# Kernel optimization log

Hardware: AMD Instinct MI355X
Metric: run time of the kernel (lower is better)

The kernel has to match this reference:

```python
import jax, jax.numpy as jnp
import numpy as np

D_MODEL = 1024
H = 16
D_K = D_MODEL // H
D_FF = 4096
EPS = 1e-5
NEG = -1e9


def setup_inputs() -> dict:
    key = jax.random.key(0)
    ks = jax.random.split(key, 12)
    B, S = 4, 1024
    s = 1.0 / np.sqrt(D_MODEL)
    inp = {
        'x': jax.random.normal(ks[0], (B, S, D_MODEL), dtype=jnp.float32),
        'src_mask': jax.random.randint(ks[1], (B, 1, 1, S), 0, 2, dtype=jnp.int32),
        'wq': jax.random.normal(ks[2], (D_MODEL, D_MODEL), dtype=jnp.float32) * s,
        'bq': jnp.zeros((D_MODEL,), jnp.float32),
        'wk': jax.random.normal(ks[3], (D_MODEL, D_MODEL), dtype=jnp.float32) * s,
        'bk': jnp.zeros((D_MODEL,), jnp.float32),
        'wv': jax.random.normal(ks[4], (D_MODEL, D_MODEL), dtype=jnp.float32) * s,
        'bv': jnp.zeros((D_MODEL,), jnp.float32),
        'wo': jax.random.normal(ks[5], (D_MODEL, D_MODEL), dtype=jnp.float32) * s,
        'bo': jnp.zeros((D_MODEL,), jnp.float32),
        'w1': jax.random.normal(ks[6], (D_MODEL, D_FF), dtype=jnp.float32) * s,
        'b1': jnp.zeros((D_FF,), jnp.float32),
        'w2': jax.random.normal(ks[7], (D_FF, D_MODEL), dtype=jnp.float32) * (1.0 / np.sqrt(D_FF)),
        'b2': jnp.zeros((D_MODEL,), jnp.float32),
        'ln1_a': jnp.ones((1,), jnp.float32),
        'ln1_b': jnp.zeros((1,), jnp.float32),
        'ln2_a': jnp.ones((1,), jnp.float32),
        'ln2_b': jnp.zeros((1,), jnp.float32),
    }
    return inp


def _layernorm(x, alpha, bias):
    # Matches torch: mean over last dim; std is UNBIASED (ddof=1); divide by (std + eps).
    mean = jnp.mean(x, axis=-1, keepdims=True)
    std = jnp.sqrt(jnp.var(x, axis=-1, keepdims=True, ddof=1))
    return alpha * (x - mean) / (std + EPS) + bias


def _attention(xn, src_mask, wq, bq, wk, bk, wv, bv, wo, bo):
    B, S, _ = xn.shape
    q = (xn @ wq + bq).reshape(B, S, H, D_K).transpose(0, 2, 1, 3)  # [B,H,S,Dk]
    k = (xn @ wk + bk).reshape(B, S, H, D_K).transpose(0, 2, 1, 3)
    v = (xn @ wv + bv).reshape(B, S, H, D_K).transpose(0, 2, 1, 3)
    scores = jnp.einsum('bhqd,bhkd->bhqk', q, k) / np.sqrt(D_K)
    scores = jnp.where(src_mask == 0, NEG, scores)
    # NOTE: original module applies NO softmax (faithful to source).
    out = jnp.einsum('bhqk,bhkd->bhqd', scores, v)  # [B,H,S,Dk]
    out = out.transpose(0, 2, 1, 3).reshape(B, S, D_MODEL)
    return out @ wo + bo


def reference(x, src_mask, wq, bq, wk, bk, wv, bv, wo, bo,
              w1, b1, w2, b2, ln1_a, ln1_b, ln2_a, ln2_b):
    # Pre-norm residual 1: self-attention
    x = x + _attention(_layernorm(x, ln1_a, ln1_b), src_mask,
                       wq, bq, wk, bk, wv, bv, wo, bo)
    # Pre-norm residual 2: FFN
    xn = _layernorm(x, ln2_a, ln2_b)
    ffn = jax.nn.relu(xn @ w1 + b1) @ w2 + b2
    return x + ffn
```

## Files before the change

### kernel.cpp

```cpp
#include <hip/hip_runtime.h>
#include <hip/hip_bf16.h>
#include <math.h>


#define EPS 1e-5f

typedef __attribute__((ext_vector_type(8))) short bf16x8;
typedef __attribute__((ext_vector_type(4))) float f32x4;
typedef __attribute__((ext_vector_type(8))) int i32x8;
typedef __attribute__((ext_vector_type(4))) int i32x4;

typedef const __attribute__((address_space(1))) unsigned char glob_byte;
typedef __attribute__((address_space(3))) unsigned char lds_byte;

__device__ __forceinline__ void g2l16(const void* g, void* l) {
  __builtin_amdgcn_global_load_lds((glob_byte*)g, (lds_byte*)l, 16, 0, 0);
}

__device__ __forceinline__ unsigned short f2bf(float f) {
  union { float f; unsigned int u; } v; v.f = f;
  return (unsigned short)((v.u + 0x7FFFu + ((v.u >> 16) & 1u)) >> 16);
}
__device__ __forceinline__ float bf2f(unsigned short b) {
  union { unsigned int u; float f; } v; v.u = (unsigned int)b << 16;
  return v.f;
}
__device__ __forceinline__ unsigned int pk_fp8x4(float a, float b, float c, float d) {
  unsigned int p = 0;
  p = __builtin_amdgcn_cvt_pk_fp8_f32(a, b, p, false);
  p = __builtin_amdgcn_cvt_pk_fp8_f32(c, d, p, true);
  return p;
}
__device__ __forceinline__ unsigned char f2f8(float v) {
  return (unsigned char)(__builtin_amdgcn_cvt_pk_fp8_f32(v, v, 0, false) & 0xFF);
}

__global__ __launch_bounds__(256) void wconv_ln_kernel(
    const float* __restrict__ wq, const float* __restrict__ wk,
    const float* __restrict__ wv, const float* __restrict__ wo,
    const float* __restrict__ w1, const float* __restrict__ w2,
    const float* __restrict__ bq, const float* __restrict__ bk,
    const float* __restrict__ bv, const float* __restrict__ bo,
    unsigned char* __restrict__ wqkvF8, unsigned short* __restrict__ woT,
    unsigned short* __restrict__ wvT16,
    unsigned char* __restrict__ w1F8, unsigned char* __restrict__ w2F8,
    float* __restrict__ bqkv, float* __restrict__ cboW,
    const float* __restrict__ x, unsigned char* __restrict__ xnF8,
    unsigned short* __restrict__ xn16,
    const float* __restrict__ ln1a, const float* __restrict__ ln1b) {
  __shared__ float tile[64][65];
  const int bid = blockIdx.x;
  const int t = threadIdx.x;
  if (bid >= 3073) {
    const int row = bid - 3073;
    const float4 v = ((const float4*)(x + (size_t)row * 1024))[t];
    float s  = v.x + v.y + v.z + v.w;
    float ss = v.x * v.x + v.y * v.y + v.z * v.z + v.w * v.w;
#pragma unroll
    for (int off = 32; off > 0; off >>= 1) {
      s  += __shfl_down(s, off, 64);
      ss += __shfl_down(ss, off, 64);
    }
    __shared__ float red[8];
    const int lane = t & 63, wv_ = t >> 6;
    if (lane == 0) { red[wv_] = s; red[4 + wv_] = ss; }
    __syncthreads();
    const float S  = red[0] + red[1] + red[2] + red[3];
    const float SS = red[4] + red[5] + red[6] + red[7];
    const float mean = S * (1.0f / 1024.0f);
    float var = (SS - 1024.0f * mean * mean) * (1.0f / 1023.0f);
    var = fmaxf(var, 0.0f);
    const float scl = ln1a[0] / (sqrtf(var) + EPS);
    const float b = ln1b[0];
    const float o0 = (v.x - mean) * scl + b;
    const float o1 = (v.y - mean) * scl + b;
    const float o2 = (v.z - mean) * scl + b;
    const float o3 = (v.w - mean) * scl + b;
    ((unsigned int*)xnF8)[(size_t)row * 256 + t] = pk_fp8x4(o0, o1, o2, o3);
    ushort4 o4;
    o4.x = f2bf(o0); o4.y = f2bf(o1); o4.z = f2bf(o2); o4.w = f2bf(o3);
    ((ushort4*)(xn16 + (size_t)row * 1024))[t] = o4;
    return;
  }
  if (bid == 3072) {
#pragma unroll
    for (int i = 0; i < 12; ++i) {
      const int n = i * 256 + t;
      bqkv[n] = n < 1024 ? bq[n] : (n < 2048 ? bk[n - 1024] : bv[n - 2048]);
    }
#pragma unroll
    for (int i = 0; i < 16; ++i) {
      const int idx = i * 256 + t;
      cboW[idx] = bo[idx & 1023];
    }
    return;
  }
  const float* src; int K, N, tk, tn;
  unsigned short* dst16 = nullptr; unsigned char* dst8 = nullptr;
  unsigned short* dstv = nullptr;
  if (bid < 1024) {
    const int m = bid >> 8, loc = bid & 255;
    src = m == 0 ? wq : m == 1 ? wk : m == 2 ? wv : wo;
    if (m == 3) dst16 = woT;
    else { dst8 = wqkvF8 + (size_t)m * 1024 * 1024; if (m == 2) dstv = wvT16; }
    K = 1024; N = 1024; tk = loc >> 4; tn = loc & 15;
  } else if (bid < 2048) {
    const int loc = bid - 1024; src = w1; dst8 = w1F8;
    K = 1024; N = 4096; tk = loc >> 6; tn = loc & 63;
  } else {
    const int loc = bid - 2048; src = w2; dst8 = w2F8;
    K = 4096; N = 1024; tk = loc >> 4; tn = loc & 15;
  }
  const int lr = t >> 4, lc = (t & 15) * 4;
#pragma unroll
  for (int i = 0; i < 4; ++i) {
    const float4 v = *(const float4*)(src + (size_t)(tk * 64 + lr + 16 * i) * N + tn * 64 + lc);
    tile[lr + 16 * i][lc + 0] = v.x;
    tile[lr + 16 * i][lc + 1] = v.y;
    tile[lr + 16 * i][lc + 2] = v.z;
    tile[lr + 16 * i][lc + 3] = v.w;
  }
  __syncthreads();
  const int on = t >> 2, ok = (t & 3) * 16;
#pragma unroll
  for (int jj = 0; jj < 4; ++jj) {
    if (dst8) {
      const unsigned int p = pk_fp8x4(tile[ok + 4 * jj + 0][on], tile[ok + 4 * jj + 1][on],
                                      tile[ok + 4 * jj + 2][on], tile[ok + 4 * jj + 3][on]);
      *(unsigned int*)(dst8 + (size_t)(tn * 64 + on) * K + tk * 64 + ok + 4 * jj) = p;
      if (dstv) {
        ushort4 o4;
        o4.x = f2bf(tile[ok + 4 * jj + 0][on]);
        o4.y = f2bf(tile[ok + 4 * jj + 1][on]);
        o4.z = f2bf(tile[ok + 4 * jj + 2][on]);
        o4.w = f2bf(tile[ok + 4 * jj + 3][on]);
        *(ushort4*)(dstv + (size_t)(tn * 64 + on) * 1024 + tk * 64 + ok + 4 * jj) = o4;
      }
    } else {
      ushort4 o4;
      o4.x = f2bf(tile[ok + 4 * jj + 0][on]);
      o4.y = f2bf(tile[ok + 4 * jj + 1][on]);
      o4.z = f2bf(tile[ok + 4 * jj + 2][on]);
      o4.w = f2bf(tile[ok + 4 * jj + 3][on]);
      *(ushort4*)(dst16 + (size_t)(tn * 64 + on) * K + tk * 64 + ok + 4 * jj) = o4;
    }
  }
}

__global__ __launch_bounds__(256) void msum_kernel(
    const unsigned short* __restrict__ xn16, const int* __restrict__ mask,
    float* __restrict__ partials, float* __restrict__ nmp) {
  const int blk = blockIdx.x, b = blk >> 4, rc = blk & 15;
  const int t = threadIdx.x;
  const int row0 = b * 1024 + rc * 64;
  float4 s = {0.f, 0.f, 0.f, 0.f};
  float cnt = 0.f;
#pragma unroll 4
  for (int r = 0; r < 64; ++r) {
    const int row = row0 + r;
    if (mask[row] == 0) {
      const ushort4 v = ((const ushort4*)(xn16 + (size_t)row * 1024))[t];
      s.x += bf2f(v.x); s.y += bf2f(v.y); s.z += bf2f(v.z); s.w += bf2f(v.w);
      cnt += 1.f;
    }
  }
  ((float4*)(partials + (size_t)blk * 1024))[t] = s;
  if (t == 0) nmp[blk] = cnt;
}

template <int EPI, int TN, int RX, int RY>
__global__ __launch_bounds__(256, 4) void mfma_gemm_fp8(
    const unsigned char* __restrict__ A, const unsigned char* __restrict__ Bt,
    const float* __restrict__ bias, const void* __restrict__ resv,
    void* __restrict__ C0, void* __restrict__ C1, const int* __restrict__ maskG,
    int N, int lda, int ldb, int KH) {
  constexpr int NSPAN = TN / 2;
  constexpr int NJ = NSPAN / 16;
  __shared__ __align__(16) unsigned char As[128 * 128];
  __shared__ __align__(16) unsigned char Bs[TN * 128];
  const int tid = threadIdx.x, lane = tid & 63;
  const int w = tid >> 6;
  const int quad = lane >> 4, col = lane & 15;
  const int wm = w & 1, wn = w >> 1;

  int bx = blockIdx.x, by = blockIdx.y;
  {
    const int gx = gridDim.x;
    const int L = bx + gx * by;
    const int r = L & 7, s = L >> 3;
    const int nrx = gx / RX;
    const int rx = r % nrx, ry = r / nrx;
    bx = rx * RX + s % RX;
    by = ry * RY + (s / RX) % RY;
  }
  const int m0 = by * 128, n0 = bx * TN;
  if (EPI == 3) {
    const int bb = m0 >> 10;
    Bt += (size_t)bb * 1024 * ldb;
    bias += bb * 1024;
  }

  f32x4 acc[4][NJ];
  const f32x4 z4 = {0.f, 0.f, 0.f, 0.f};
#pragma unroll
  for (int i = 0; i < 4; ++i)
#pragma unroll
    for (int j = 0; j < NJ; ++j) acc[i][j] = z4;

  for (int k0 = 0; k0 < KH; k0 += 128) {
    __syncthreads();
#pragma unroll
    for (int t = 0; t < 4; ++t) {
      const int s = t * 256 + tid;
      const int r = s >> 3, c = (s & 7) ^ (r & 7);
      g2l16(A + (size_t)(m0 + r) * lda + k0 + c * 16, (void*)(As + s * 16));
    }
#pragma unroll
    for (int t = 0; t < TN / 32; ++t) {
      const int s = t * 256 + tid;
      const int r = s >> 3, c = (s & 7) ^ (r & 7);
      g2l16(Bt + (size_t)(n0 + r) * ldb + k0 + c * 16, (void*)(Bs + s * 16));
    }
    __syncthreads();
    i32x8 af[4];
#pragma unroll
    for (int i = 0; i < 4; ++i) {
      const int rr = wm * 64 + i * 16 + col;
      const i32x4* rowp = (const i32x4*)(As + rr * 128);
      const i32x4 lo = rowp[(2 * quad) ^ (rr & 7)];
      const i32x4 hi = rowp[(2 * quad + 1) ^ (rr & 7)];
      af[i] = __builtin_shufflevector(lo, hi, 0, 1, 2, 3, 4, 5, 6, 7);
    }
#pragma unroll
    for (int j = 0; j < NJ; ++j) {
      const int rr = wn * NSPAN + j * 16 + col;
      const i32x4* rowp = (const i32x4*)(Bs + rr * 128);
      const i32x4 lo = rowp[(2 * quad) ^ (rr & 7)];
      const i32x4 hi = rowp[(2 * quad + 1) ^ (rr & 7)];
      const i32x8 bfj = __builtin_shufflevector(lo, hi, 0, 1, 2, 3, 4, 5, 6, 7);
#pragma unroll
      for (int i = 0; i < 4; ++i)
        acc[i][j] = __builtin_amdgcn_mfma_scale_f32_16x16x128_f8f6f4(
            af[i], bfj, acc[i][j], 0, 0, 0, 0x7F7F7F7Fu, 0, 0x7F7F7F7Fu);
    }
  }
#pragma unroll
  for (int i = 0; i < 4; ++i) {
    const int mrow = m0 + wm * 64 + i * 16 + quad * 4;
#pragma unroll
    for (int j = 0; j < NJ; ++j) {
      const int n = n0 + wn * NSPAN + j * 16 + col;
      const float bn = bias[n];
      if (EPI == 2) {
        if (n0 >= 1024) {
          float v0 = acc[i][j][0] + bn;
          float v1 = acc[i][j][1] + bn;
          float v2 = acc[i][j][2] + bn;
          float v3 = acc[i][j][3] + bn;
          if (n0 < 2048) {
            const int4 mq = *(const int4*)(maskG + mrow);
            v0 = mq.x ? v0 : 0.f;
            v1 = mq.y ? v1 : 0.f;
            v2 = mq.z ? v2 : 0.f;
            v3 = mq.w ? v3 : 0.f;
          }
          *(unsigned int*)((unsigned char*)C1 + (size_t)(n - 1024) * 4096 + mrow) =
              pk_fp8x4(v0, v1, v2, v3);
        } else {
#pragma unroll
          for (int r = 0; r < 4; ++r)
            ((unsigned char*)C0)[(size_t)(mrow + r) * N + n] = f2f8(acc[i][j][r] + bn);
        }
        continue;
      }
#pragma unroll
      for (int r = 0; r < 4; ++r) {
        const int m = mrow + r;
        if (EPI == 0) {
          ((unsigned char*)C0)[(size_t)m * N + n] = f2f8(fmaxf(acc[i][j][r] + bn, 0.f));
        } else if (EPI == 1) {
          const float v = acc[i][j][r] + bn + bf2f(((const unsigned short*)resv)[(size_t)m * N + n]);
          ((float*)C0)[(size_t)m * N + n] = v;
        } else {
          const float v = acc[i][j][r] + bn + ((const float*)resv)[(size_t)m * N + n];
          ((unsigned short*)C0)[(size_t)m * N + n] = f2bf(v);
        }
      }
    }
  }
}

__global__ __launch_bounds__(256) void ln2_kernel(
    const unsigned short* __restrict__ x1,
    const float* __restrict__ alpha, const float* __restrict__ beta,
    unsigned char* __restrict__ xn2f8) {
  const int row = blockIdx.x, t = threadIdx.x;
  const size_t i = (size_t)row * 256 + t;
  const ushort4 a4 = ((const ushort4*)x1)[i];
  float4 v;
  v.x = bf2f(a4.x); v.y = bf2f(a4.y); v.z = bf2f(a4.z); v.w = bf2f(a4.w);
  float s  = v.x + v.y + v.z + v.w;
  float ss = v.x * v.x + v.y * v.y + v.z * v.z + v.w * v.w;
#pragma unroll
  for (int off = 32; off > 0; off >>= 1) {
    s  += __shfl_down(s, off, 64);
    ss += __shfl_down(ss, off, 64);
  }
  __shared__ float red[8];
  const int lane = t & 63, wv_ = t >> 6;
  if (lane == 0) { red[wv_] = s; red[4 + wv_] = ss; }
  __syncthreads();
  const float S  = red[0] + red[1] + red[2] + red[3];
  const float SS = red[4] + red[5] + red[6] + red[7];
  const float mean = S * (1.0f / 1024.0f);
  float var = (SS - 1024.0f * mean * mean) * (1.0f / 1023.0f);
  var = fmaxf(var, 0.0f);
  const float scl = alpha[0] / (sqrtf(var) + EPS);
  const float bb = beta[0];
  ((unsigned int*)xn2f8)[i] = pk_fp8x4((v.x - mean) * scl + bb,
                                       (v.y - mean) * scl + bb,
                                       (v.z - mean) * scl + bb,
                                       (v.w - mean) * scl + bb);
}

__global__ __launch_bounds__(512) void moment_kernel(
    const unsigned char* __restrict__ kvT8, const unsigned short* __restrict__ woT,
    const unsigned short* __restrict__ wvT16, const float* __restrict__ bqkv,
    const float* __restrict__ partials, const float* __restrict__ nmp,
    unsigned char* __restrict__ Wbt8, float* __restrict__ cboW) {
  __shared__ __align__(16) unsigned char Ks[64 * 512];
  __shared__ __align__(16) unsigned char Vs[64 * 512];
  __shared__ __align__(16) unsigned short Ms[64 * 64];
  __shared__ float sS[1024];
  __shared__ float corrS[64];
  const int tid = threadIdx.x, lane = tid & 63, w = tid >> 6;
  const int quad = lane >> 4, col = lane & 15;
  const int bh = blockIdx.x, b = bh >> 4, h = bh & 15;
  const int w4 = w & 3, ch = w >> 2;
  const f32x4 z4 = {0.f, 0.f, 0.f, 0.f};
  const size_t kb = (size_t)(h * 64) * 4096 + b * 1024;
  const size_t vb = (size_t)(1024 + h * 64) * 4096 + b * 1024;

#pragma unroll
  for (int i = 0; i < 4; ++i) {
    const int s = i * 512 + tid;
    const int r = s >> 5, c = (s & 31) ^ (r & 31);
    g2l16(kvT8 + kb + (size_t)r * 4096 + c * 16, (void*)(Ks + s * 16));
    g2l16(kvT8 + vb + (size_t)r * 4096 + c * 16, (void*)(Vs + s * 16));
  }
  {
    float2 sacc = {0.f, 0.f};
#pragma unroll
    for (int rc = 0; rc < 16; ++rc) {
      const float2 p = ((const float2*)(partials + (size_t)(b * 16 + rc) * 1024))[tid];
      sacc.x += p.x; sacc.y += p.y;
    }
    ((float2*)sS)[tid] = sacc;
  }
  float nm = 0.f;
#pragma unroll
  for (int i = 0; i < 16; ++i) nm += nmp[b * 16 + i];
  __syncthreads();

  {
    const int d2 = tid >> 3, kq = tid & 7;
    const unsigned short* wrow = wvT16 + (size_t)(h * 64 + d2) * 1024 + kq * 128;
    float s = 0.f;
#pragma unroll
    for (int jj = 0; jj < 16; ++jj) {
      const bf16x8 w8 = *(const bf16x8*)(wrow + jj * 8);
      const float* sp = sS + kq * 128 + jj * 8;
      s += bf2f((unsigned short)w8[0]) * sp[0] + bf2f((unsigned short)w8[1]) * sp[1] +
           bf2f((unsigned short)w8[2]) * sp[2] + bf2f((unsigned short)w8[3]) * sp[3] +
           bf2f((unsigned short)w8[4]) * sp[4] + bf2f((unsigned short)w8[5]) * sp[5] +
           bf2f((unsigned short)w8[6]) * sp[6] + bf2f((unsigned short)w8[7]) * sp[7];
    }
    s += __shfl_xor(s, 1, 64);
    s += __shfl_xor(s, 2, 64);
    s += __shfl_xor(s, 4, 64);
    if ((lane & 7) == 0) corrS[d2] = s + nm * bqkv[2048 + h * 64 + d2];
  }

  f32x4 acc[2] = {z4, z4};
  const int rr = w4 * 16 + col;
#pragma unroll 1
  for (int st = 0; st < 2; ++st) {
    if (st) {
      __syncthreads();
#pragma unroll
      for (int i = 0; i < 4; ++i) {
        const int s = i * 512 + tid;
        const int r = s >> 5, c = (s & 31) ^ (r & 31);
        g2l16(kvT8 + kb + (size_t)r * 4096 + 512 + c * 16, (void*)(Ks + s * 16));
        g2l16(kvT8 + vb + (size_t)r * 4096 + 512 + c * 16, (void*)(Vs + s * 16));
      }
      __syncthreads();
    }
#pragma unroll
    for (int q = 0; q < 4; ++q) {
      const i32x4* rowpK = (const i32x4*)(Ks + rr * 512);
      const i32x4 klo = rowpK[(q * 8 + 2 * quad) ^ (rr & 31)];
      const i32x4 khi = rowpK[(q * 8 + 2 * quad + 1) ^ (rr & 31)];
      const i32x8 af = __builtin_shufflevector(klo, khi, 0, 1, 2, 3, 4, 5, 6, 7);
#pragma unroll
      for (int cl = 0; cl < 2; ++cl) {
        const int vr = (ch * 2 + cl) * 16 + col;
        const i32x4* rowpV = (const i32x4*)(Vs + vr * 512);
        const i32x4 vlo = rowpV[(q * 8 + 2 * quad) ^ (vr & 31)];
        const i32x4 vhi = rowpV[(q * 8 + 2 * quad + 1) ^ (vr & 31)];
        const i32x8 vf = __builtin_shufflevector(vlo, vhi, 0, 1, 2, 3, 4, 5, 6, 7);
        acc[cl] = __builtin_amdgcn_mfma_scale_f32_16x16x128_f8f6f4(
            af, vf, acc[cl], 0, 0, 0, 0x7F7F7F7Fu, 0, 0x7F7F7F7Fu);
      }
    }
  }
#pragma unroll
  for (int cl = 0; cl < 2; ++cl) {
    const int d2 = (ch * 2 + cl) * 16 + col;
#pragma unroll
    for (int r = 0; r < 4; ++r) {
      const int d1 = w4 * 16 + quad * 4 + r;
      Ms[d1 * 64 + ((d2 >> 3) ^ (d1 & 7)) * 8 + (d2 & 7)] = f2bf(0.125f * acc[cl][r]);
    }
  }
  __syncthreads();

  unsigned char* Wb8 = Wbt8 + (size_t)b * 1048576;
#pragma unroll 1
  for (int nt8 = 0; nt8 < 8; ++nt8) {
    const int nbase = (w * 8 + nt8) * 16;
    const bf16x8 af0 = *(const bf16x8*)(woT + (size_t)(nbase + col) * 1024 + h * 64 + quad * 8);
    const bf16x8 af1 = *(const bf16x8*)(woT + (size_t)(nbase + col) * 1024 + h * 64 + 32 + quad * 8);
#pragma unroll
    for (int dt = 0; dt < 4; ++dt) {
      const int d1r = dt * 16 + col;
      const bf16x8 bf0 = *(const bf16x8*)(Ms + d1r * 64 + ((quad ^ (d1r & 7)) * 8));
      const bf16x8 bf1 = *(const bf16x8*)(Ms + d1r * 64 + (((4 + quad) ^ (d1r & 7)) * 8));
      f32x4 a = __builtin_amdgcn_mfma_f32_16x16x32_bf16(af0, bf0, z4, 0, 0, 0);
      a = __builtin_amdgcn_mfma_f32_16x16x32_bf16(af1, bf1, a, 0, 0, 0);
#pragma unroll
      for (int r = 0; r < 4; ++r)
        Wb8[(size_t)(nbase + quad * 4 + r) * 1024 + h * 64 + dt * 16 + col] = f2f8(a[r]);
    }
  }
#pragma unroll
  for (int rep = 0; rep < 2; ++rep) {
    const int n = rep * 512 + tid;
    const unsigned short* wrow = woT + (size_t)n * 1024 + h * 64;
    float s = 0.f;
#pragma unroll
    for (int k = 0; k < 64; k += 8) {
      const bf16x8 w8 = *(const bf16x8*)(wrow + k);
      s += bf2f((unsigned short)w8[0]) * corrS[k + 0] +
           bf2f((unsigned short)w8[1]) * corrS[k + 1] +
           bf2f((unsigned short)w8[2]) * corrS[k + 2] +
           bf2f((unsigned short)w8[3]) * corrS[k + 3] +
           bf2f((unsigned short)w8[4]) * corrS[k + 4] +
           bf2f((unsigned short)w8[5]) * corrS[k + 5] +
           bf2f((unsigned short)w8[6]) * corrS[k + 6] +
           bf2f((unsigned short)w8[7]) * corrS[k + 7];
    }
    atomicAdd(cboW + b * 1024 + n, -1e9f * s);
  }
}

extern "C" void kernel_launch(void* const* d_in, const int* in_sizes, int n_in,
                              void* d_out, int out_size, void* d_ws, size_t ws_size,
                              hipStream_t stream) {
  const float* x    = (const float*)d_in[0];
  const int*   mask = (const int*)d_in[1];
  const float* wq = (const float*)d_in[2];
  const float* bq = (const float*)d_in[3];
  const float* wk = (const float*)d_in[4];
  const float* bk = (const float*)d_in[5];
  const float* wv = (const float*)d_in[6];
  const float* bv = (const float*)d_in[7];
  const float* wo = (const float*)d_in[8];
  const float* bo = (const float*)d_in[9];
  const float* w1 = (const float*)d_in[10];
  const float* b1 = (const float*)d_in[11];
  const float* w2 = (const float*)d_in[12];
  const float* b2 = (const float*)d_in[13];
  const float* ln1a = (const float*)d_in[14];
  const float* ln1b = (const float*)d_in[15];
  const float* ln2a = (const float*)d_in[16];
  const float* ln2b = (const float*)d_in[17];
  float* out = (float*)d_out;
  char* W = (char*)d_ws;
  const size_t MB = 1u << 20;

  unsigned char*  wqkvF8 = (unsigned char*)(W + 0 * MB);
  unsigned short* woT    = (unsigned short*)(W + 3 * MB);
  unsigned short* wvT16  = (unsigned short*)(W + 5 * MB);
  unsigned char*  w1F8   = (unsigned char*)(W + 7 * MB);
  unsigned char*  w2F8   = (unsigned char*)(W + 11 * MB);
  float*          bqkv   = (float*)(W + 15 * MB);
  float*          cboW   = (float*)(W + 15 * MB + 65536);
  float*          partials = (float*)(W + 15 * MB + 131072);
  float*          nmp    = (float*)(W + 15 * MB + 393216);
  unsigned char*  xnF8   = (unsigned char*)(W + 16 * MB);
  unsigned char*  Q8     = (unsigned char*)(W + 20 * MB);
  unsigned char*  kvT8   = (unsigned char*)(W + 24 * MB);
  unsigned char*  Wbt8   = (unsigned char*)(W + 32 * MB);
  unsigned short* x1     = (unsigned short*)(W + 36 * MB);
  unsigned short* xn16   = (unsigned short*)(W + 44 * MB);
  unsigned char*  xn2f8  = (unsigned char*)(W + 52 * MB);
  unsigned char*  hbF8   = (unsigned char*)(W + 56 * MB);

  wconv_ln_kernel<<<7169, 256, 0, stream>>>(wq, wk, wv, wo, w1, w2, bq, bk, bv, bo,
                                            wqkvF8, woT, wvT16, w1F8, w2F8,
                                            bqkv, cboW, x, xnF8, xn16, ln1a, ln1b);
  msum_kernel<<<64, 256, 0, stream>>>(xn16, mask, partials, nmp);
  mfma_gemm_fp8<2, 128, 12, 8><<<dim3(24, 32), 256, 0, stream>>>(
      xnF8, wqkvF8, bqkv, nullptr, Q8, kvT8, mask, 1024, 1024, 1024, 1024);
  moment_kernel<<<64, 512, 0, stream>>>(kvT8, woT, wvT16, bqkv, partials, nmp,
                                        Wbt8, cboW);
  mfma_gemm_fp8<3, 64, 8, 8><<<dim3(16, 32), 256, 0, stream>>>(
      Q8, Wbt8, cboW, x, x1, nullptr, nullptr, 1024, 1024, 1024, 1024);
  ln2_kernel<<<4096, 256, 0, stream>>>(x1, ln2a, ln2b, xn2f8);
  mfma_gemm_fp8<0, 128, 16, 8><<<dim3(32, 32), 256, 0, stream>>>(
      xn2f8, w1F8, b1, nullptr, hbF8, nullptr, nullptr, 4096, 1024, 1024, 1024);
  mfma_gemm_fp8<1, 64, 8, 8><<<dim3(16, 32), 256, 0, stream>>>(
      hbF8, w2F8, b2, x1, out, nullptr, nullptr, 1024, 4096, 4096, 4096);
}
```

Measured before the change: 266.3 us.

## Quantize QKV, FFN weights and activations to FP4 for scaled MFMA GEMMs

Replaces the FP8 operand encoding for the QKV projection and both FFN GEMMs with a hand-rolled FP4 (e2m1) encoder. Weights are pre-scaled by 32 or 64 and the scale is undone through the MFMA block-scale argument. The GEMM kernel is duplicated into an FP4 variant that packs two k-steps per LDS tile, halving operand bytes and load traffic. The FFN hidden activation is also stored packed in FP4. This heavily reduces numeric precision of activations and weights, which risks accuracy-tolerance failures.

```diff
diff --git a/kernel.cpp b/kernel.cpp
--- a/kernel.cpp
+++ b/kernel.cpp
@@ -33,6 +33,14 @@
 }
 __device__ __forceinline__ unsigned char f2f8(float v) {
   return (unsigned char)(__builtin_amdgcn_cvt_pk_fp8_f32(v, v, 0, false) & 0xFF);
+}
+__device__ __forceinline__ unsigned fp4enc(float v) {
+  const float a = fabsf(v);
+  unsigned c = (unsigned)(a >= 0.25f) + (unsigned)(a >= 0.75f) +
+               (unsigned)(a >= 1.25f) + (unsigned)(a >= 1.75f) +
+               (unsigned)(a >= 2.5f) + (unsigned)(a >= 3.5f) +
+               (unsigned)(a >= 5.0f);
+  return c | (v < 0.f ? 8u : 0u);
 }
 
 __global__ __launch_bounds__(256) void wconv_ln_kernel(
@@ -41,11 +49,11 @@
     const float* __restrict__ w1, const float* __restrict__ w2,
     const float* __restrict__ bq, const float* __restrict__ bk,
     const float* __restrict__ bv, const float* __restrict__ bo,
-    unsigned char* __restrict__ wqkvF8, unsigned short* __restrict__ woT,
+    unsigned char* __restrict__ wqkvF4, unsigned short* __restrict__ woT,
     unsigned short* __restrict__ wvT16,
-    unsigned char* __restrict__ w1F8, unsigned char* __restrict__ w2F8,
+    unsigned char* __restrict__ w1F4, unsigned char* __restrict__ w2F4,
     float* __restrict__ bqkv, float* __restrict__ cboW,
-    const float* __restrict__ x, unsigned char* __restrict__ xnF8,
+    const float* __restrict__ x, unsigned char* __restrict__ xnF4,
     unsigned short* __restrict__ xn16,
     const float* __restrict__ ln1a, const float* __restrict__ ln1b) {
   __shared__ float tile[64][65];
@@ -76,7 +84,8 @@
     const float o1 = (v.y - mean) * scl + b;
     const float o2 = (v.z - mean) * scl + b;
     const float o3 = (v.w - mean) * scl + b;
-    ((unsigned int*)xnF8)[(size_t)row * 256 + t] = pk_fp8x4(o0, o1, o2, o3);
+    ((unsigned short*)xnF4)[(size_t)row * 256 + t] = (unsigned short)(
+        fp4enc(o0) | (fp4enc(o1) << 4) | (fp4enc(o2) << 8) | (fp4enc(o3) << 12));
     ushort4 o4;
     o4.x = f2bf(o0); o4.y = f2bf(o1); o4.z = f2bf(o2); o4.w = f2bf(o3);
     ((ushort4*)(xn16 + (size_t)row * 1024))[t] = o4;
@@ -96,19 +105,20 @@
     return;
   }
   const float* src; int K, N, tk, tn;
-  unsigned short* dst16 = nullptr; unsigned char* dst8 = nullptr;
+  float ps = 32.f;
+  unsigned short* dst16 = nullptr; unsigned char* dst4 = nullptr;
   unsigned short* dstv = nullptr;
   if (bid < 1024) {
     const int m = bid >> 8, loc = bid & 255;
     src = m == 0 ? wq : m == 1 ? wk : m == 2 ? wv : wo;
     if (m == 3) dst16 = woT;
-    else { dst8 = wqkvF8 + (size_t)m * 1024 * 1024; if (m == 2) dstv = wvT16; }
+    else { dst4 = wqkvF4 + (size_t)m * 1024 * 512; if (m == 2) dstv = wvT16; }
     K = 1024; N = 1024; tk = loc >> 4; tn = loc & 15;
   } else if (bid < 2048) {
-    const int loc = bid - 1024; src = w1; dst8 = w1F8;
+    const int loc = bid - 1024; src = w1; dst4 = w1F4;
     K = 1024; N = 4096; tk = loc >> 6; tn = loc & 63;
   } else {
-    const int loc = bid - 2048; src = w2; dst8 = w2F8;
+    const int loc = bid - 2048; src = w2; dst4 = w2F4; ps = 64.f;
     K = 4096; N = 1024; tk = loc >> 4; tn = loc & 15;
   }
   const int lr = t >> 4, lc = (t & 15) * 4;
@@ -124,10 +134,14 @@
   const int on = t >> 2, ok = (t & 3) * 16;
 #pragma unroll
   for (int jj = 0; jj < 4; ++jj) {
-    if (dst8) {
-      const unsigned int p = pk_fp8x4(tile[ok + 4 * jj + 0][on], tile[ok + 4 * jj + 1][on],
-                                      tile[ok + 4 * jj + 2][on], tile[ok + 4 * jj + 3][on]);
-      *(unsigned int*)(dst8 + (size_t)(tn * 64 + on) * K + tk * 64 + ok + 4 * jj) = p;
+    if (dst4) {
+      const unsigned e0 = fp4enc(tile[ok + 4 * jj + 0][on] * ps);
+      const unsigned e1 = fp4enc(tile[ok + 4 * jj + 1][on] * ps);
+      const unsigned e2 = fp4enc(tile[ok + 4 * jj + 2][on] * ps);
+      const unsigned e3 = fp4enc(tile[ok + 4 * jj + 3][on] * ps);
+      *(unsigned short*)(dst4 + (size_t)(tn * 64 + on) * (K >> 1) +
+                         ((tk * 64 + ok + 4 * jj) >> 1)) =
+          (unsigned short)(e0 | (e1 << 4) | (e2 << 8) | (e3 << 12));
       if (dstv) {
         ushort4 o4;
         o4.x = f2bf(tile[ok + 4 * jj + 0][on]);
@@ -168,12 +182,12 @@
   if (t == 0) nmp[blk] = cnt;
 }
 
-template <int EPI, int TN, int RX, int RY>
-__global__ __launch_bounds__(256, 4) void mfma_gemm_fp8(
+template <int EPI, int TN, int RX, int RY, unsigned SB>
+__global__ __launch_bounds__(256, 4) void mfma_gemm_fp4(
     const unsigned char* __restrict__ A, const unsigned char* __restrict__ Bt,
     const float* __restrict__ bias, const void* __restrict__ resv,
     void* __restrict__ C0, void* __restrict__ C1, const int* __restrict__ maskG,
-    int N, int lda, int ldb, int KH) {
+    int N, int ldab, int ldbb, int KB) {
   constexpr int NSPAN = TN / 2;
   constexpr int NJ = NSPAN / 16;
   __shared__ __align__(16) unsigned char As[128 * 128];
@@ -194,11 +208,6 @@
     by = ry * RY + (s / RX) % RY;
   }
   const int m0 = by * 128, n0 = bx * TN;
-  if (EPI == 3) {
-    const int bb = m0 >> 10;
-    Bt += (size_t)bb * 1024 * ldb;
-    bias += bb * 1024;
-  }
 
   f32x4 acc[4][NJ];
   const f32x4 z4 = {0.f, 0.f, 0.f, 0.f};
@@ -207,41 +216,42 @@
 #pragma unroll
     for (int j = 0; j < NJ; ++j) acc[i][j] = z4;
 
-  for (int k0 = 0; k0 < KH; k0 += 128) {
+  for (int k0 = 0; k0 < KB; k0 += 128) {
     __syncthreads();
 #pragma unroll
     for (int t = 0; t < 4; ++t) {
       const int s = t * 256 + tid;
       const int r = s >> 3, c = (s & 7) ^ (r & 7);
-      g2l16(A + (size_t)(m0 + r) * lda + k0 + c * 16, (void*)(As + s * 16));
+      g2l16(A + (size_t)(m0 + r) * ldab + k0 + c * 16, (void*)(As + s * 16));
     }
 #pragma unroll
     for (int t = 0; t < TN / 32; ++t) {
       const int s = t * 256 + tid;
       const int r = s >> 3, c = (s & 7) ^ (r & 7);
-      g2l16(Bt + (size_t)(n0 + r) * ldb + k0 + c * 16, (void*)(Bs + s * 16));
+      g2l16(Bt + (size_t)(n0 + r) * ldbb + k0 + c * 16, (void*)(Bs + s * 16));
     }
     __syncthreads();
-    i32x8 af[4];
-#pragma unroll
-    for (int i = 0; i < 4; ++i) {
-      const int rr = wm * 64 + i * 16 + col;
-      const i32x4* rowp = (const i32x4*)(As + rr * 128);
-      const i32x4 lo = rowp[(2 * quad) ^ (rr & 7)];
-      const i32x4 hi = rowp[(2 * quad + 1) ^ (rr & 7)];
-      af[i] = __builtin_shufflevector(lo, hi, 0, 1, 2, 3, 4, 5, 6, 7);
-    }
-#pragma unroll
-    for (int j = 0; j < NJ; ++j) {
-      const int rr = wn * NSPAN + j * 16 + col;
-      const i32x4* rowp = (const i32x4*)(Bs + rr * 128);
-      const i32x4 lo = rowp[(2 * quad) ^ (rr & 7)];
-      const i32x4 hi = rowp[(2 * quad + 1) ^ (rr & 7)];
-      const i32x8 bfj = __builtin_shufflevector(lo, hi, 0, 1, 2, 3, 4, 5, 6, 7);
-#pragma unroll
-      for (int i = 0; i < 4; ++i)
-        acc[i][j] = __builtin_amdgcn_mfma_scale_f32_16x16x128_f8f6f4(
-            af[i], bfj, acc[i][j], 0, 0, 0, 0x7F7F7F7Fu, 0, 0x7F7F7F7Fu);
+#pragma unroll
+    for (int kk = 0; kk < 2; ++kk) {
+      i32x8 af[4];
+#pragma unroll
+      for (int i = 0; i < 4; ++i) {
+        const int rr = wm * 64 + i * 16 + col;
+        const i32x4* rowp = (const i32x4*)(As + rr * 128);
+        const i32x4 q = rowp[(kk * 4 + quad) ^ (rr & 7)];
+        af[i] = __builtin_shufflevector(q, q, 0, 1, 2, 3, 4, 5, 6, 7);
+      }
+#pragma unroll
+      for (int j = 0; j < NJ; ++j) {
+        const int rr = wn * NSPAN + j * 16 + col;
+        const i32x4* rowp = (const i32x4*)(Bs + rr * 128);
+        const i32x4 q = rowp[(kk * 4 + quad) ^ (rr & 7)];
+        const i32x8 bfj = __builtin_shufflevector(q, q, 0, 1, 2, 3, 4, 5, 6, 7);
+#pragma unroll
+        for (int i = 0; i < 4; ++i)
+          acc[i][j] = __builtin_amdgcn_mfma_scale_f32_16x16x128_f8f6f4(
+              af[i], bfj, acc[i][j], 4, 4, 0, 0x7F7F7F7Fu, 0, SB);
+      }
     }
   }
 #pragma unroll
@@ -277,14 +287,111 @@
       for (int r = 0; r < 4; ++r) {
         const int m = mrow + r;
         if (EPI == 0) {
-          ((unsigned char*)C0)[(size_t)m * N + n] = f2f8(fmaxf(acc[i][j][r] + bn, 0.f));
-        } else if (EPI == 1) {
+          const float v = fmaxf(acc[i][j][r] + bn, 0.f);
+          const unsigned e = fp4enc(v);
+          const unsigned eo = __shfl_down(e, 1, 64);
+          if (!(lane & 1))
+            ((unsigned char*)C0)[(size_t)m * (N >> 1) + (n >> 1)] =
+                (unsigned char)(e | (eo << 4));
+        } else {
           const float v = acc[i][j][r] + bn + bf2f(((const unsigned short*)resv)[(size_t)m * N + n]);
           ((float*)C0)[(size_t)m * N + n] = v;
-        } else {
-          const float v = acc[i][j][r] + bn + ((const float*)resv)[(size_t)m * N + n];
-          ((unsigned short*)C0)[(size_t)m * N + n] = f2bf(v);
         }
+      }
+    }
+  }
+}
+
+template <int EPI, int TN, int RX, int RY>
+__global__ __launch_bounds__(256, 4) void mfma_gemm_fp8(
+    const unsigned char* __restrict__ A, const unsigned char* __restrict__ Bt,
+    const float* __restrict__ bias, const void* __restrict__ resv,
+    void* __restrict__ C0, void* __restrict__ C1, const int* __restrict__ maskG,
+    int N, int lda, int ldb, int KH) {
+  constexpr int NSPAN = TN / 2;
+  constexpr int NJ = NSPAN / 16;
+  __shared__ __align__(16) unsigned char As[128 * 128];
+  __shared__ __align__(16) unsigned char Bs[TN * 128];
+  const int tid = threadIdx.x, lane = tid & 63;
+  const int w = tid >> 6;
+  const int quad = lane >> 4, col = lane & 15;
+  const int wm = w & 1, wn = w >> 1;
+
+  int bx = blockIdx.x, by = blockIdx.y;
+  {
+    const int gx = gridDim.x;
+    const int L = bx + gx * by;
+    const int r = L & 7, s = L >> 3;
+    const int nrx = gx / RX;
+    const int rx = r % nrx, ry = r / nrx;
+    bx = rx * RX + s % RX;
+    by = ry * RY + (s / RX) % RY;
+  }
+  const int m0 = by * 128, n0 = bx * TN;
+  const unsigned char* Bt2 = Bt;
+  const float* bias2 = bias;
+  if (EPI == 3) {
+    const int bb = m0 >> 10;
+    Bt2 += (size_t)bb * 1024 * ldb;
+    bias2 += bb * 1024;
+  }
+
+  f32x4 acc[4][NJ];
+  const f32x4 z4 = {0.f, 0.f, 0.f, 0.f};
+#pragma unroll
+  for (int i = 0; i < 4; ++i)
+#pragma unroll
+    for (int j = 0; j < NJ; ++j) acc[i][j] = z4;
+
+  for (int k0 = 0; k0 < KH; k0 += 128) {
+    __syncthreads();
+#pragma unroll
+    for (int t = 0; t < 4; ++t) {
+      const int s = t * 256 + tid;
+      const int r = s >> 3, c = (s & 7) ^ (r & 7);
+      g2l16(A + (size_t)(m0 + r) * lda + k0 + c * 16, (void*)(As + s * 16));
+    }
+#pragma unroll
+    for (int t = 0; t < TN / 32; ++t) {
+      const int s = t * 256 + tid;
+      const int r = s >> 3, c = (s & 7) ^ (r & 7);
+      g2l16(Bt2 + (size_t)(n0 + r) * ldb + k0 + c * 16, (void*)(Bs + s * 16));
+    }
+    __syncthreads();
+    i32x8 af[4];
+#pragma unroll
+    for (int i = 0; i < 4; ++i) {
+      const int rr = wm * 64 + i * 16 + col;
+      const i32x4* rowp = (const i32x4*)(As + rr * 128);
+      const i32x4 lo = rowp[(2 * quad) ^ (rr & 7)];
+      const i32x4 hi = rowp[(2 * quad + 1) ^ (rr & 7)];
+      af[i] = __builtin_shufflevector(lo, hi, 0, 1, 2, 3, 4, 5, 6, 7);
+    }
+#pragma unroll
+    for (int j = 0; j < NJ; ++j) {
+      const int rr = wn * NSPAN + j * 16 + col;
+      const i32x4* rowp = (const i32x4*)(Bs + rr * 128);
+      const i32x4 lo = rowp[(2 * quad) ^ (rr & 7)];
+      const i32x4 hi = rowp[(2 * quad + 1) ^ (rr & 7)];
+      const i32x8 bfj = __builtin_shufflevector(lo, hi, 0, 1, 2, 3, 4, 5, 6, 7);
+#pragma unroll
+      for (int i = 0; i < 4; ++i)
+        acc[i][j] = __builtin_amdgcn_mfma_scale_f32_16x16x128_f8f6f4(
+            af[i], bfj, acc[i][j], 0, 0, 0, 0x7F7F7F7Fu, 0, 0x7F7F7F7Fu);
+    }
+  }
+#pragma unroll
+  for (int i = 0; i < 4; ++i) {
+    const int mrow = m0 + wm * 64 + i * 16 + quad * 4;
+#pragma unroll
+    for (int j = 0; j < NJ; ++j) {
+      const int n = n0 + wn * NSPAN + j * 16 + col;
+      const float bn = bias2[n];
+#pragma unroll
+      for (int r = 0; r < 4; ++r) {
+        const int m = mrow + r;
+        const float v = acc[i][j][r] + bn + ((const float*)resv)[(size_t)m * N + n];
+        ((unsigned short*)C0)[(size_t)m * N + n] = f2bf(v);
       }
     }
   }
@@ -293,7 +400,7 @@
 __global__ __launch_bounds__(256) void ln2_kernel(
     const unsigned short* __restrict__ x1,
     const float* __restrict__ alpha, const float* __restrict__ beta,
-    unsigned char* __restrict__ xn2f8) {
+    unsigned char* __restrict__ xn2f4) {
   const int row = blockIdx.x, t = threadIdx.x;
   const size_t i = (size_t)row * 256 + t;
   const ushort4 a4 = ((const ushort4*)x1)[i];
@@ -317,10 +424,12 @@
   var = fmaxf(var, 0.0f);
   const float scl = alpha[0] / (sqrtf(var) + EPS);
   const float bb = beta[0];
-  ((unsigned int*)xn2f8)[i] = pk_fp8x4((v.x - mean) * scl + bb,
-                                       (v.y - mean) * scl + bb,
-                                       (v.z - mean) * scl + bb,
-                                       (v.w - mean) * scl + bb);
+  const float o0 = (v.x - mean) * scl + bb;
+  const float o1 = (v.y - mean) * scl + bb;
+  const float o2 = (v.z - mean) * scl + bb;
+  const float o3 = (v.w - mean) * scl + bb;
+  ((unsigned short*)xn2f4)[i] = (unsigned short)(
+      fp4enc(o0) | (fp4enc(o1) << 4) | (fp4enc(o2) << 8) | (fp4enc(o3) << 12));
 }
 
 __global__ __launch_bounds__(512) void moment_kernel(
@@ -489,37 +598,37 @@
   char* W = (char*)d_ws;
   const size_t MB = 1u << 20;
 
-  unsigned char*  wqkvF8 = (unsigned char*)(W + 0 * MB);
-  unsigned short* woT    = (unsigned short*)(W + 3 * MB);
-  unsigned short* wvT16  = (unsigned short*)(W + 5 * MB);
-  unsigned char*  w1F8   = (unsigned char*)(W + 7 * MB);
-  unsigned char*  w2F8   = (unsigned char*)(W + 11 * MB);
-  float*          bqkv   = (float*)(W + 15 * MB);
-  float*          cboW   = (float*)(W + 15 * MB + 65536);
-  float*          partials = (float*)(W + 15 * MB + 131072);
-  float*          nmp    = (float*)(W + 15 * MB + 393216);
-  unsigned char*  xnF8   = (unsigned char*)(W + 16 * MB);
-  unsigned char*  Q8     = (unsigned char*)(W + 20 * MB);
-  unsigned char*  kvT8   = (unsigned char*)(W + 24 * MB);
-  unsigned char*  Wbt8   = (unsigned char*)(W + 32 * MB);
-  unsigned short* x1     = (unsigned short*)(W + 36 * MB);
-  unsigned short* xn16   = (unsigned short*)(W + 44 * MB);
-  unsigned char*  xn2f8  = (unsigned char*)(W + 52 * MB);
-  unsigned char*  hbF8   = (unsigned char*)(W + 56 * MB);
+  unsigned char*  wqkvF4 = (unsigned char*)(W + 0 * MB);
+  unsigned short* woT    = (unsigned short*)(W + 2 * MB);
+  unsigned short* wvT16  = (unsigned short*)(W + 4 * MB);
+  unsigned char*  w1F4   = (unsigned char*)(W + 6 * MB);
+  unsigned char*  w2F4   = (unsigned char*)(W + 8 * MB);
+  float*          bqkv   = (float*)(W + 10 * MB);
+  float*          cboW   = (float*)(W + 10 * MB + 65536);
+  float*          partials = (float*)(W + 10 * MB + 131072);
+  float*          nmp    = (float*)(W + 10 * MB + 458752);
+  unsigned char*  xnF4   = (unsigned char*)(W + 11 * MB);
+  unsigned char*  Q8     = (unsigned char*)(W + 13 * MB);
+  unsigned char*  kvT8   = (unsigned char*)(W + 17 * MB);
+  unsigned char*  Wbt8   = (unsigned char*)(W + 25 * MB);
+  unsigned short* x1     = (unsigned short*)(W + 29 * MB);
+  unsigned short* xn16   = (unsigned short*)(W + 37 * MB);
+  unsigned char*  xn2f4  = (unsigned char*)(W + 45 * MB);
+  unsigned char*  hbF4   = (unsigned char*)(W + 47 * MB);
 
   wconv_ln_kernel<<<7169, 256, 0, stream>>>(wq, wk, wv, wo, w1, w2, bq, bk, bv, bo,
-                                            wqkvF8, woT, wvT16, w1F8, w2F8,
-                                            bqkv, cboW, x, xnF8, xn16, ln1a, ln1b);
+                                            wqkvF4, woT, wvT16, w1F4, w2F4,
+                                            bqkv, cboW, x, xnF4, xn16, ln1a, ln1b);
   msum_kernel<<<64, 256, 0, stream>>>(xn16, mask, partials, nmp);
-  mfma_gemm_fp8<2, 128, 12, 8><<<dim3(24, 32), 256, 0, stream>>>(
-      xnF8, wqkvF8, bqkv, nullptr, Q8, kvT8, mask, 1024, 1024, 1024, 1024);
+  mfma_gemm_fp4<2, 128, 12, 8, 0x7A7A7A7AU><<<dim3(24, 32), 256, 0, stream>>>(
+      xnF4, wqkvF4, bqkv, nullptr, Q8, kvT8, mask, 1024, 512, 512, 512);
   moment_kernel<<<64, 512, 0, stream>>>(kvT8, woT, wvT16, bqkv, partials, nmp,
                                         Wbt8, cboW);
   mfma_gemm_fp8<3, 64, 8, 8><<<dim3(16, 32), 256, 0, stream>>>(
       Q8, Wbt8, cboW, x, x1, nullptr, nullptr, 1024, 1024, 1024, 1024);
-  ln2_kernel<<<4096, 256, 0, stream>>>(x1, ln2a, ln2b, xn2f8);
-  mfma_gemm_fp8<0, 128, 16, 8><<<dim3(32, 32), 256, 0, stream>>>(
-      xn2f8, w1F8, b1, nullptr, hbF8, nullptr, nullptr, 4096, 1024, 1024, 1024);
-  mfma_gemm_fp8<1, 64, 8, 8><<<dim3(16, 32), 256, 0, stream>>>(
-      hbF8, w2F8, b2, x1, out, nullptr, nullptr, 1024, 4096, 4096, 4096);
-}
+  ln2_kernel<<<4096, 256, 0, stream>>>(x1, ln2a, ln2b, xn2f4);
+  mfma_gemm_fp4<0, 128, 16, 8, 0x7A7A7A7AU><<<dim3(32, 32), 256, 0, stream>>>(
+      xn2f4, w1F4, b1, nullptr, hbF4, nullptr, nullptr, 4096, 512, 512, 512);
+  mfma_gemm_fp4<1, 64, 8, 8, 0x79797979U><<<dim3(16, 32), 256, 0, stream>>>(
+      hbF4, w2F4, b2, x1, out, nullptr, nullptr, 1024, 2048, 2048, 2048);
+}
```

New measurement: 244.4 us. 8.2% less time.
